# Performance work log

Hardware: AMD Instinct MI355X
Metric: run time of the kernel (lower is better)

The kernel has to match this reference:

```python
import jax, jax.numpy as jnp
import numpy as np

NS = 4  # ns_mesh hard-coded to [4,4,4] in the original forward


def _interp_weights(positions, cell):
    """Order-3 (M3) B-spline interpolation weights and periodic mesh indices.

    Returns w27 (N,27) combined weights and lin (N,27) flat mesh indices.
    """
    frac = positions @ jnp.linalg.inv(cell)          # fractional coords (N,3)
    u = frac * NS
    nearest = jnp.floor(u + 0.5)
    x = u - nearest                                   # in [-0.5, 0.5]
    # order-3 assignment weights at offsets -1, 0, +1
    w = jnp.stack([0.5 * (0.5 - x) ** 2,
                   0.75 - x ** 2,
                   0.5 * (0.5 + x) ** 2], axis=-1)    # (N,3dims,3offs)
    offs = jnp.array([-1, 0, 1], dtype=jnp.int32)
    idx = (nearest[..., None].astype(jnp.int32) + offs) % NS  # (N,3,3)
    w27 = (w[:, 0, :, None, None] * w[:, 1, None, :, None] * w[:, 2, None, None, :]
           ).reshape(-1, 27)
    lin = (idx[:, 0, :, None, None] * NS * NS
           + idx[:, 1, None, :, None] * NS
           + idx[:, 2, None, None, :]).reshape(-1, 27)
    return w27, lin


def _kspace_filter(cell, sigma2):
    """Smeared-Coulomb kernel exp(-k^2 sigma2/2)/k^2 on the rfft half-grid."""
    G = 2.0 * jnp.pi * jnp.linalg.inv(cell).T         # reciprocal lattice rows
    fx = jnp.fft.fftfreq(NS) * NS                     # integer frequencies
    fz = jnp.fft.rfftfreq(NS) * NS
    kvec = (fx[:, None, None, None] * G[0]
            + fx[None, :, None, None] * G[1]
            + fz[None, None, :, None] * G[2])         # (NS,NS,NS//2+1,3)
    k2 = jnp.sum(kvec ** 2, axis=-1)
    k2_safe = jnp.where(k2 > 0, k2, 1.0)
    return jnp.where(k2 > 0, jnp.exp(-k2 * sigma2 * 0.5) / k2_safe, 0.0)


def reference(positions, cell, charges, sigma2, W1, b1, W2, b2, W3, b3):
    w27, lin = _interp_weights(positions, cell)       # (N,27) each
    C = charges.shape[1]
    # points_to_mesh: scatter-add charges with stencil weights
    contrib = (w27[:, :, None] * charges[:, None, :]).reshape(-1, C)
    mesh_flat = jnp.zeros((NS ** 3, C), charges.dtype).at[lin.reshape(-1)].add(contrib)
    mesh = mesh_flat.T.reshape(C, NS, NS, NS)
    # k-space filter: rfft (backward norm) -> multiply -> irfft (forward norm)
    kernel = _kspace_filter(cell, sigma2)
    mesh_hat = jnp.fft.rfftn(mesh, axes=(1, 2, 3))
    mesh = jnp.fft.irfftn(mesh_hat * kernel, s=(NS, NS, NS), axes=(1, 2, 3),
                          norm="forward")
    # mesh_to_points: gather with the same stencil weights
    mesh_flat = mesh.reshape(C, -1).T                 # (NS^3, C)
    pot = jnp.sum(mesh_flat[lin] * w27[:, :, None], axis=1)  # (N,C)
    # tiny MLP on [charge, potential]
    x = jnp.concatenate([charges, pot], axis=1)       # (N,2)
    x = jnp.tanh(x @ W1 + b1)
    x = jnp.tanh(x @ W2 + b2)
    return jnp.sum(x @ W3 + b3)


def setup_inputs() -> dict:
    key = jax.random.key(0)
    ks = jax.random.split(key, 8)
    N = 2_000_000
    L = 6.0
    positions = jax.random.uniform(ks[0], (N, 3), dtype=jnp.float32) * L
    cell = jnp.eye(3, dtype=jnp.float32) * L
    charges = jax.random.normal(ks[1], (N, 1), dtype=jnp.float32)
    sigma2 = jnp.asarray(1.0, dtype=jnp.float32)
    s1, s2, s3 = (1.0 / np.sqrt(2), 1.0 / np.sqrt(10), 1.0 / np.sqrt(10))
    W1 = jax.random.normal(ks[2], (2, 10), jnp.float32) * s1
    b1 = jnp.zeros((10,), jnp.float32)
    W2 = jax.random.normal(ks[3], (10, 10), jnp.float32) * s2
    b2 = jnp.zeros((10,), jnp.float32)
    W3 = jax.random.normal(ks[4], (10, 1), jnp.float32) * s3
    b3 = jnp.zeros((1,), jnp.float32)
    return {"positions": positions, "cell": cell, "charges": charges,
            "sigma2": sigma2, "W1": W1, "b1": b1, "W2": W2, "b2": b2,
            "W3": W3, "b3": b3}
```

## Files before the change

### kernel.cpp

```cpp
#include <hip/hip_runtime.h>
#include <math.h>

#define NSM 4
#define NCELL 64
#define R1_BLOCKS 64

typedef float f32x2 __attribute__((ext_vector_type(2)));

#define TANH_SC 2.8853900817779268f


__device__ __forceinline__ f32x2 splat2(float s) { f32x2 v; v.x = s; v.y = s; return v; }

__device__ __forceinline__ f32x2 pkfma(f32x2 a, f32x2 b, f32x2 c) {
#if __has_builtin(__builtin_elementwise_fma)
    return __builtin_elementwise_fma(a, b, c);
#else
    f32x2 r; r.x = fmaf(a.x, b.x, c.x); r.y = fmaf(a.y, b.y, c.y); return r;
#endif
}

__device__ __forceinline__ float fast_exp2(float x) {
#if __has_builtin(__builtin_amdgcn_exp2f)
    return __builtin_amdgcn_exp2f(x);
#else
    return exp2f(x);
#endif
}

__device__ __forceinline__ void inv3x3(const float* __restrict__ C, float* inv) {
    float a=C[0],b=C[1],c=C[2],d=C[3],e=C[4],f=C[5],g=C[6],h=C[7],i=C[8];
    float A  =  (e*i - f*h);
    float B  = -(d*i - f*g);
    float Cc =  (d*h - e*g);
    float det = a*A + b*B + c*Cc;
    float rd = 1.0f/det;
    inv[0] = A*rd;        inv[1] = (c*h - b*i)*rd; inv[2] = (b*f - c*e)*rd;
    inv[3] = B*rd;        inv[4] = (a*i - c*g)*rd; inv[5] = (c*d - a*f)*rd;
    inv[6] = Cc*rd;       inv[7] = (b*g - a*h)*rd; inv[8] = (a*e - b*d)*rd;
}

struct AxW { float wm, w0, wp; int n; };
__device__ __forceinline__ AxW axw(float u) {
    AxW r;
    float nf = rintf(u);
    float x  = u - nf;
    r.w0 = 0.75f - x*x;
    float tm = 0.5f - x;  r.wm = 0.5f*tm*tm;
    float tp = 0.5f + x;  r.wp = 0.5f*tp*tp;
    r.n = ((int)nf) & 3;
    return r;
}

__device__ __forceinline__ void axis_w4(float u, float* __restrict__ W) {
    AxW a = axw(u);
    #pragma unroll
    for (int j = 0; j < 4; j++) {
        float w = (a.n == j)         ? a.w0 : 0.0f;
        w       = (a.n == ((j+1)&3)) ? a.wm : w;
        w       = (a.n == ((j+3)&3)) ? a.wp : w;
        W[j] = w;
    }
}

__device__ __forceinline__ float tanh1(float x) {
    float e = fast_exp2(x * TANH_SC);
    return fmaf(-2.0f, __builtin_amdgcn_rcpf(e + 1.0f), 1.0f);
}
__device__ __forceinline__ f32x2 tanh2v(f32x2 v) {
    float e0 = fast_exp2(v.x * TANH_SC);
    float e1 = fast_exp2(v.y * TANH_SC);
    f32x2 r;
    r.x = fmaf(-2.0f, __builtin_amdgcn_rcpf(e0 + 1.0f), 1.0f);
    r.y = fmaf(-2.0f, __builtin_amdgcn_rcpf(e1 + 1.0f), 1.0f);
    return r;
}


__device__ __forceinline__ void scatter_one(float px, float py, float pz, float q,
                                            const float* __restrict__ ci,
                                            f32x2* __restrict__ macc) {
    float fx = px*ci[0] + py*ci[3] + pz*ci[6];
    float fy = px*ci[1] + py*ci[4] + pz*ci[7];
    float fz = px*ci[2] + py*ci[5] + pz*ci[8];
    float X[4], Y[4], Z[4];
    axis_w4(fx*(float)NSM, X);
    axis_w4(fy*(float)NSM, Y);
    axis_w4(fz*(float)NSM, Z);
    f32x2 z01; z01.x = Z[0]; z01.y = Z[1];
    f32x2 z23; z23.x = Z[2]; z23.y = Z[3];
    float qX[4];
    #pragma unroll
    for (int x = 0; x < 4; x++) qX[x] = q * X[x];
    #pragma unroll
    for (int x = 0; x < 4; x++) {
        #pragma unroll
        for (int y = 0; y < 4; y++) {
            f32x2 w2 = splat2(qX[x] * Y[y]);
            macc[x*8 + y*2    ] = pkfma(w2, z01, macc[x*8 + y*2    ]);
            macc[x*8 + y*2 + 1] = pkfma(w2, z23, macc[x*8 + y*2 + 1]);
        }
    }
}

__global__ __launch_bounds__(256) void scatter_kernel(
        const float* __restrict__ pos, const float* __restrict__ cell,
        const float* __restrict__ charges, float* __restrict__ partial, int N) {
    __shared__ f32x2 red[128][32];
    __shared__ f32x2 red2[8][32];
    float ci[9]; inv3x3(cell, ci);

    f32x2 macc[32];
    #pragma unroll
    for (int c = 0; c < 32; c++) macc[c] = splat2(0.0f);

    const float4* posv = (const float4*)pos;
    const float4* qv   = (const float4*)charges;
    long b = (long)blockIdx.x * blockDim.x + threadIdx.x;
    long i = b * 4;
    if (i + 3 < N) {
        float4 p0 = posv[3*b], p1 = posv[3*b+1], p2 = posv[3*b+2];
        float4 q4 = qv[b];
        scatter_one(p0.x, p0.y, p0.z, q4.x, ci, macc);
        scatter_one(p0.w, p1.x, p1.y, q4.y, ci, macc);
        scatter_one(p1.z, p1.w, p2.x, q4.z, ci, macc);
        scatter_one(p2.y, p2.z, p2.w, q4.w, ci, macc);
    } else if (i < N) {
        for (long k = i; k < N; k++)
            scatter_one(pos[3*k], pos[3*k+1], pos[3*k+2], charges[k], ci, macc);
    }

    #pragma unroll
    for (int c = 0; c < 32; c++) {
        macc[c].x += __shfl_xor(macc[c].x, 32);
        macc[c].y += __shfl_xor(macc[c].y, 32);
    }
    int t = threadIdx.x;
    int row = (t >> 6) * 32 + (t & 31);
    if ((t & 32) == 0) {
        int sw = t & 31;
        #pragma unroll
        for (int c = 0; c < 32; c++) red[row][c ^ sw] = macc[c];
    }
    __syncthreads();
    {
        int p = t & 31, g = t >> 5;
        f32x2 sum = splat2(0.0f);
        #pragma unroll
        for (int i2 = 0; i2 < 16; i2++) {
            int r = g*16 + i2;
            sum += red[r][p ^ (r & 31)];
        }
        red2[g][p] = sum;
    }
    __syncthreads();
    if (t < NCELL) {
        const float* r2 = (const float*)&red2[0][0];
        int pair = t >> 1, comp = t & 1;
        float s = 0.0f;
        #pragma unroll
        for (int gg = 0; gg < 8; gg++) s += r2[(gg*32 + pair)*2 + comp];
        partial[(long)blockIdx.x * NCELL + t] = s;
    }
}


__global__ __launch_bounds__(256) void reduce_stage1_kernel(
        const float* __restrict__ partial, int nb, float* __restrict__ partial2) {
    __shared__ float acc[4][64];
    int t = threadIdx.x;
    int c = t & 63, g = t >> 6;
    float s = 0.0f;
    for (int r = blockIdx.x + 64*g; r < nb; r += 256)
        s += partial[(long)r * NCELL + c];
    acc[g][c] = s;
    __syncthreads();
    if (t < 64) {
        float v = ((acc[0][t] + acc[1][t]) + acc[2][t]) + acc[3][t];
        partial2[(long)blockIdx.x * NCELL + t] = v;
    }
}


__global__ __launch_bounds__(256) void reduce_filter_kernel(
        const float* __restrict__ partial2,
        const float* __restrict__ cell, const float* __restrict__ sigma2p,
        float* __restrict__ mesh_out) {
    __shared__ float4 redA[16][16];
    __shared__ float mm[64];
    __shared__ float gr[64];
    int t = threadIdx.x;

    int c4 = t & 15, g = t >> 4;
    float4 v = make_float4(0.f, 0.f, 0.f, 0.f);
    const float4* p4 = (const float4*)partial2;
    for (int b = g; b < R1_BLOCKS; b += 16) {
        float4 x = p4[b*16 + c4];
        v.x += x.x; v.y += x.y; v.z += x.z; v.w += x.w;
    }
    redA[g][c4] = v;
    __syncthreads();
    if (t < 16) {
        float4 tot = make_float4(0.f, 0.f, 0.f, 0.f);
        #pragma unroll
        for (int gg = 0; gg < 16; gg++) {
            float4 x = redA[gg][t];
            tot.x += x.x; tot.y += x.y; tot.z += x.z; tot.w += x.w;
        }
        ((float4*)mm)[t] = tot;
    }
    __syncthreads();

    if (t < 64) {
        float ci[9]; inv3x3(cell, ci);
        float s2 = sigma2p[0];
        const float twopi = 6.2831853071795864769f;
        float G0x = twopi*ci[0], G0y = twopi*ci[3], G0z = twopi*ci[6];
        float G1x = twopi*ci[1], G1y = twopi*ci[4], G1z = twopi*ci[7];
        float G2x = twopi*ci[2], G2y = twopi*ci[5], G2z = twopi*ci[8];
        int dx = t >> 4, dy = (t >> 2) & 3, dz = t & 3;
        float acc = 0.0f;
        for (int a = 0; a < 4; a++) {
            float fa = (a < 2) ? (float)a : (float)(a - 4);
            for (int b = 0; b < 4; b++) {
                float fb = (b < 2) ? (float)b : (float)(b - 4);
                for (int c = 0; c < 4; c++) {
                    if ((a | b | c) == 0) continue;
                    float fc = (c < 2) ? (float)c : (float)(c - 4);
                    float kx = fa*G0x + fb*G1x + fc*G2x;
                    float ky = fa*G0y + fb*G1y + fc*G2y;
                    float kz = fa*G0z + fb*G1z + fc*G2z;
                    float k2 = kx*kx + ky*ky + kz*kz;
                    float K  = expf(-k2 * s2 * 0.5f) / k2;
                    int ph = (a*dx + b*dy + c*dz) & 3;
                    float cs = (ph == 0) ? 1.0f : ((ph == 2) ? -1.0f : 0.0f);
                    acc += K * cs;
                }
            }
        }
        gr[t] = acc;
    }
    __syncthreads();
    if (t < 64) {
        int dx = t >> 4, dy = (t >> 2) & 3, dz = t & 3;
        float o = 0.0f;
        for (int s = 0; s < 64; s++) {
            int sx = s >> 4, sy = (s >> 2) & 3, sz = s & 3;
            int d = ((dx - sx) & 3)*16 + ((dy - sy) & 3)*4 + ((dz - sz) & 3);
            o += gr[d] * mm[s];
        }
        mesh_out[t] = o;
    }
}


__device__ __forceinline__ float pot_one(float px, float py, float pz,
                                         const float* __restrict__ ci,
                                         const float* __restrict__ mf) {
    float fx = px*ci[0] + py*ci[3] + pz*ci[6];
    float fy = px*ci[1] + py*ci[4] + pz*ci[7];
    float fz = px*ci[2] + py*ci[5] + pz*ci[8];
    float X[4], Y[4], Z[4];
    axis_w4(fx*(float)NSM, X);
    axis_w4(fy*(float)NSM, Y);
    axis_w4(fz*(float)NSM, Z);
    f32x2 a01 = splat2(0.0f), a23 = splat2(0.0f);
    #pragma unroll
    for (int x = 0; x < 4; x++) {
        #pragma unroll
        for (int y = 0; y < 4; y++) {
            f32x2 w2 = splat2(X[x] * Y[y]);
            f32x2 m01, m23;
            m01.x = mf[x*16 + y*4 + 0]; m01.y = mf[x*16 + y*4 + 1];
            m23.x = mf[x*16 + y*4 + 2]; m23.y = mf[x*16 + y*4 + 3];
            a01 = pkfma(w2, m01, a01);
            a23 = pkfma(w2, m23, a23);
        }
    }
    return a01.x*Z[0] + a01.y*Z[1] + a23.x*Z[2] + a23.y*Z[3];
}

__global__ __launch_bounds__(256, 4) void gather_mlp_kernel(
        const float* __restrict__ pos, const float* __restrict__ cell,
        const float* __restrict__ charges,
        const float* __restrict__ W1, const float* __restrict__ b1,
        const float* __restrict__ W2, const float* __restrict__ b2,
        const float* __restrict__ W3, const float* __restrict__ b3,
        const float* __restrict__ meshf, float* __restrict__ bsum, int N) {
    __shared__ float wavesum[4];
    int t = threadIdx.x;
    float ci[9]; inv3x3(cell, ci);

    long t4 = (long)blockIdx.x * blockDim.x + threadIdx.x;
    long i0 = t4 * 4;
    float ysum = 0.0f;

    if (i0 + 3 < N) {
        const float4* posv = (const float4*)pos;
        float4 p0 = posv[3*t4], p1 = posv[3*t4+1], p2 = posv[3*t4+2];
        float4 q4 = ((const float4*)charges)[t4];

        float pt0 = pot_one(p0.x, p0.y, p0.z, ci, meshf);
        float pt1 = pot_one(p0.w, p1.x, p1.y, ci, meshf);
        float pt2 = pot_one(p1.z, p1.w, p2.x, ci, meshf);
        float pt3 = pot_one(p2.y, p2.z, p2.w, ci, meshf);

        f32x2 q01; q01.x = q4.x; q01.y = q4.y;
        f32x2 q23; q23.x = q4.z; q23.y = q4.w;
        f32x2 pA;  pA.x = pt0;  pA.y = pt1;
        f32x2 pB;  pB.x = pt2;  pB.y = pt3;

        f32x2 h1a[10], h1b[10];
        #pragma unroll
        for (int j = 0; j < 10; j++) {
            f32x2 ta = pkfma(pA, splat2(W1[10 + j]), splat2(b1[j]));
            ta = pkfma(q01, splat2(W1[j]), ta);
            h1a[j] = tanh2v(ta);
            f32x2 tb = pkfma(pB, splat2(W1[10 + j]), splat2(b1[j]));
            tb = pkfma(q23, splat2(W1[j]), tb);
            h1b[j] = tanh2v(tb);
        }
        f32x2 h2a[10], h2b[10];
        #pragma unroll
        for (int j = 0; j < 10; j++) {
            f32x2 aa = splat2(b2[j]), ab = splat2(b2[j]);
            #pragma unroll
            for (int i = 0; i < 10; i++) {
                f32x2 w = splat2(W2[10*i + j]);
                aa = pkfma(h1a[i], w, aa);
                ab = pkfma(h1b[i], w, ab);
            }
            h2a[j] = tanh2v(aa);
            h2b[j] = tanh2v(ab);
        }
        f32x2 ya = splat2(b3[0]), yb = splat2(b3[0]);
        #pragma unroll
        for (int j = 0; j < 10; j++) {
            f32x2 w = splat2(W3[j]);
            ya = pkfma(h2a[j], w, ya);
            yb = pkfma(h2b[j], w, yb);
        }
        ysum = ya.x + ya.y + yb.x + yb.y;
    } else if (i0 < N) {
        for (long k = i0; k < N; k++) {
            float pt = pot_one(pos[3*k], pos[3*k+1], pos[3*k+2], ci, meshf);
            float q  = charges[k];
            float h1[10], h2[10];
            #pragma unroll
            for (int j = 0; j < 10; j++)
                h1[j] = tanh1(fmaf(q, W1[j], fmaf(pt, W1[10 + j], b1[j])));
            #pragma unroll
            for (int j = 0; j < 10; j++) {
                float a2 = b2[j];
                #pragma unroll
                for (int i = 0; i < 10; i++) a2 = fmaf(h1[i], W2[10*i + j], a2);
                h2[j] = tanh1(a2);
            }
            float y = b3[0];
            #pragma unroll
            for (int j = 0; j < 10; j++) y = fmaf(h2[j], W3[j], y);
            ysum += y;
        }
    }

    ysum += __shfl_down(ysum, 32);
    ysum += __shfl_down(ysum, 16);
    ysum += __shfl_down(ysum, 8);
    ysum += __shfl_down(ysum, 4);
    ysum += __shfl_down(ysum, 2);
    ysum += __shfl_down(ysum, 1);
    int wid  = t >> 6;
    int lane = t & 63;
    if (lane == 0) wavesum[wid] = ysum;
    __syncthreads();
    if (t == 0)
        bsum[blockIdx.x] = wavesum[0] + wavesum[1] + wavesum[2] + wavesum[3];
}


__global__ __launch_bounds__(256) void final_sum_kernel(
        const float* __restrict__ bsum, int nb, float* __restrict__ out) {
    __shared__ float wavesum[4];
    float s = 0.0f;
    for (int i = threadIdx.x; i < nb; i += 256) s += bsum[i];
    s += __shfl_down(s, 32);
    s += __shfl_down(s, 16);
    s += __shfl_down(s, 8);
    s += __shfl_down(s, 4);
    s += __shfl_down(s, 2);
    s += __shfl_down(s, 1);
    int wid  = threadIdx.x >> 6;
    int lane = threadIdx.x & 63;
    if (lane == 0) wavesum[wid] = s;
    __syncthreads();
    if (threadIdx.x == 0)
        out[0] = wavesum[0] + wavesum[1] + wavesum[2] + wavesum[3];
}


extern "C" void kernel_launch(void* const* d_in, const int* in_sizes, int n_in,
                              void* d_out, int out_size, void* d_ws, size_t ws_size,
                              hipStream_t stream) {
    const float* pos     = (const float*)d_in[0];
    const float* cell    = (const float*)d_in[1];
    const float* charges = (const float*)d_in[2];
    const float* sigma2  = (const float*)d_in[3];
    const float* W1 = (const float*)d_in[4];
    const float* b1 = (const float*)d_in[5];
    const float* W2 = (const float*)d_in[6];
    const float* b2 = (const float*)d_in[7];
    const float* W3 = (const float*)d_in[8];
    const float* b3 = (const float*)d_in[9];
    int N = in_sizes[2];

    int nblocks = (int)(((long)N + 1023) / 1024);

    float* partial  = (float*)d_ws;
    float* partial2 = partial + (long)nblocks * NCELL;
    float* meshf    = partial2 + (long)R1_BLOCKS * NCELL;
    float* bsum     = meshf + NCELL;

    scatter_kernel<<<nblocks, 256, 0, stream>>>(pos, cell, charges, partial, N);
    reduce_stage1_kernel<<<R1_BLOCKS, 256, 0, stream>>>(partial, nblocks, partial2);
    reduce_filter_kernel<<<1, 256, 0, stream>>>(partial2, cell, sigma2, meshf);
    gather_mlp_kernel<<<nblocks, 256, 0, stream>>>(pos, cell, charges,
                                                   W1, b1, W2, b2, W3, b3,
                                                   meshf, bsum, N);
    final_sum_kernel<<<1, 256, 0, stream>>>(bsum, nblocks, (float*)d_out);
}
```

Before: 54.83 us.

## Halve scatter blocks and fuse two-stage partial reduction into filter kernel

The scatter kernel now processes two groups of four points per thread through a grid-stride loop. This halves the number of per-block partial meshes. The separate reduce_stage1 kernel is removed, and a single 1024-thread block sums the partials directly, computing the k-space Green's function in parallel on another wavefront. This removes one kernel launch and an intermediate buffer round trip. The cost is that one block serially reduces about a thousand partial rows, and each scatter thread runs longer.

```diff
diff --git a/kernel.cpp b/kernel.cpp
--- a/kernel.cpp
+++ b/kernel.cpp
@@ -3,7 +3,6 @@
 
 #define NSM 4
 #define NCELL 64
-#define R1_BLOCKS 64
 
 typedef float f32x2 __attribute__((ext_vector_type(2)));
 
@@ -116,18 +115,25 @@
 
     const float4* posv = (const float4*)pos;
     const float4* qv   = (const float4*)charges;
-    long b = (long)blockIdx.x * blockDim.x + threadIdx.x;
-    long i = b * 4;
-    if (i + 3 < N) {
-        float4 p0 = posv[3*b], p1 = posv[3*b+1], p2 = posv[3*b+2];
-        float4 q4 = qv[b];
-        scatter_one(p0.x, p0.y, p0.z, q4.x, ci, macc);
-        scatter_one(p0.w, p1.x, p1.y, q4.y, ci, macc);
-        scatter_one(p1.z, p1.w, p2.x, q4.z, ci, macc);
-        scatter_one(p2.y, p2.z, p2.w, q4.w, ci, macc);
-    } else if (i < N) {
-        for (long k = i; k < N; k++)
-            scatter_one(pos[3*k], pos[3*k+1], pos[3*k+2], charges[k], ci, macc);
+    long NB4    = ((long)N + 3) / 4;
+    long stride = (long)gridDim.x * blockDim.x;
+
+    #pragma unroll
+    for (int pass = 0; pass < 2; pass++) {
+        long b = (long)blockIdx.x * blockDim.x + threadIdx.x + pass * stride;
+        if (b >= NB4) break;
+        long i = b * 4;
+        if (i + 3 < N) {
+            float4 p0 = posv[3*b], p1 = posv[3*b+1], p2 = posv[3*b+2];
+            float4 q4 = qv[b];
+            scatter_one(p0.x, p0.y, p0.z, q4.x, ci, macc);
+            scatter_one(p0.w, p1.x, p1.y, q4.y, ci, macc);
+            scatter_one(p1.z, p1.w, p2.x, q4.z, ci, macc);
+            scatter_one(p2.y, p2.z, p2.w, q4.w, ci, macc);
+        } else {
+            for (long k = i; k < N; k++)
+                scatter_one(pos[3*k], pos[3*k+1], pos[3*k+2], charges[k], ci, macc);
+        }
     }
 
     #pragma unroll
@@ -165,89 +171,66 @@
 }
 
 
-__global__ __launch_bounds__(256) void reduce_stage1_kernel(
-        const float* __restrict__ partial, int nb, float* __restrict__ partial2) {
-    __shared__ float acc[4][64];
-    int t = threadIdx.x;
-    int c = t & 63, g = t >> 6;
-    float s = 0.0f;
-    for (int r = blockIdx.x + 64*g; r < nb; r += 256)
-        s += partial[(long)r * NCELL + c];
-    acc[g][c] = s;
-    __syncthreads();
-    if (t < 64) {
-        float v = ((acc[0][t] + acc[1][t]) + acc[2][t]) + acc[3][t];
-        partial2[(long)blockIdx.x * NCELL + t] = v;
-    }
-}
-
-
-__global__ __launch_bounds__(256) void reduce_filter_kernel(
-        const float* __restrict__ partial2,
+__global__ __launch_bounds__(1024) void reduce_filter_kernel(
+        const float* __restrict__ partial, int nb,
         const float* __restrict__ cell, const float* __restrict__ sigma2p,
         float* __restrict__ mesh_out) {
-    __shared__ float4 redA[16][16];
+    __shared__ float acc[16][64];
     __shared__ float mm[64];
     __shared__ float gr[64];
     int t = threadIdx.x;
-
-    int c4 = t & 15, g = t >> 4;
-    float4 v = make_float4(0.f, 0.f, 0.f, 0.f);
-    const float4* p4 = (const float4*)partial2;
-    for (int b = g; b < R1_BLOCKS; b += 16) {
-        float4 x = p4[b*16 + c4];
-        v.x += x.x; v.y += x.y; v.z += x.z; v.w += x.w;
-    }
-    redA[g][c4] = v;
-    __syncthreads();
-    if (t < 16) {
-        float4 tot = make_float4(0.f, 0.f, 0.f, 0.f);
-        #pragma unroll
-        for (int gg = 0; gg < 16; gg++) {
-            float4 x = redA[gg][t];
-            tot.x += x.x; tot.y += x.y; tot.z += x.z; tot.w += x.w;
-        }
-        ((float4*)mm)[t] = tot;
-    }
-    __syncthreads();
-
-    if (t < 64) {
+    int c = t & 63, g = t >> 6;
+
+    float s = 0.0f;
+    for (int r = g; r < nb; r += 16)
+        s += partial[(long)r * NCELL + c];
+    acc[g][c] = s;
+
+    if (t >= 64 && t < 128) {
+        int tt = t - 64;
         float ci[9]; inv3x3(cell, ci);
         float s2 = sigma2p[0];
         const float twopi = 6.2831853071795864769f;
         float G0x = twopi*ci[0], G0y = twopi*ci[3], G0z = twopi*ci[6];
         float G1x = twopi*ci[1], G1y = twopi*ci[4], G1z = twopi*ci[7];
         float G2x = twopi*ci[2], G2y = twopi*ci[5], G2z = twopi*ci[8];
-        int dx = t >> 4, dy = (t >> 2) & 3, dz = t & 3;
-        float acc = 0.0f;
+        int dx = tt >> 4, dy = (tt >> 2) & 3, dz = tt & 3;
+        float accg = 0.0f;
         for (int a = 0; a < 4; a++) {
             float fa = (a < 2) ? (float)a : (float)(a - 4);
             for (int b = 0; b < 4; b++) {
                 float fb = (b < 2) ? (float)b : (float)(b - 4);
-                for (int c = 0; c < 4; c++) {
-                    if ((a | b | c) == 0) continue;
-                    float fc = (c < 2) ? (float)c : (float)(c - 4);
+                for (int cc = 0; cc < 4; cc++) {
+                    if ((a | b | cc) == 0) continue;
+                    float fc = (cc < 2) ? (float)cc : (float)(cc - 4);
                     float kx = fa*G0x + fb*G1x + fc*G2x;
                     float ky = fa*G0y + fb*G1y + fc*G2y;
                     float kz = fa*G0z + fb*G1z + fc*G2z;
                     float k2 = kx*kx + ky*ky + kz*kz;
                     float K  = expf(-k2 * s2 * 0.5f) / k2;
-                    int ph = (a*dx + b*dy + c*dz) & 3;
+                    int ph = (a*dx + b*dy + cc*dz) & 3;
                     float cs = (ph == 0) ? 1.0f : ((ph == 2) ? -1.0f : 0.0f);
-                    acc += K * cs;
+                    accg += K * cs;
                 }
             }
         }
-        gr[t] = acc;
+        gr[tt] = accg;
+    }
+    __syncthreads();
+    if (t < 64) {
+        float v = 0.0f;
+        #pragma unroll
+        for (int gg = 0; gg < 16; gg++) v += acc[gg][t];
+        mm[t] = v;
     }
     __syncthreads();
     if (t < 64) {
         int dx = t >> 4, dy = (t >> 2) & 3, dz = t & 3;
         float o = 0.0f;
-        for (int s = 0; s < 64; s++) {
-            int sx = s >> 4, sy = (s >> 2) & 3, sz = s & 3;
+        for (int s2i = 0; s2i < 64; s2i++) {
+            int sx = s2i >> 4, sy = (s2i >> 2) & 3, sz = s2i & 3;
             int d = ((dx - sx) & 3)*16 + ((dy - sy) & 3)*4 + ((dz - sz) & 3);
-            o += gr[d] * mm[s];
+            o += gr[d] * mm[s2i];
         }
         mesh_out[t] = o;
     }
@@ -413,18 +396,18 @@
     const float* b3 = (const float*)d_in[9];
     int N = in_sizes[2];
 
-    int nblocks = (int)(((long)N + 1023) / 1024);
-
-    float* partial  = (float*)d_ws;
-    float* partial2 = partial + (long)nblocks * NCELL;
-    float* meshf    = partial2 + (long)R1_BLOCKS * NCELL;
-    float* bsum     = meshf + NCELL;
-
-    scatter_kernel<<<nblocks, 256, 0, stream>>>(pos, cell, charges, partial, N);
-    reduce_stage1_kernel<<<R1_BLOCKS, 256, 0, stream>>>(partial, nblocks, partial2);
-    reduce_filter_kernel<<<1, 256, 0, stream>>>(partial2, cell, sigma2, meshf);
-    gather_mlp_kernel<<<nblocks, 256, 0, stream>>>(pos, cell, charges,
-                                                   W1, b1, W2, b2, W3, b3,
-                                                   meshf, bsum, N);
-    final_sum_kernel<<<1, 256, 0, stream>>>(bsum, nblocks, (float*)d_out);
-}
+    int sc_blocks = (int)(((long)N + 2047) / 2048);
+    int ga_blocks = (int)(((long)N + 1023) / 1024);
+
+    float* partial = (float*)d_ws;
+    float* meshf   = partial + (long)sc_blocks * NCELL;
+    float* bsum    = meshf + NCELL;
+
+    scatter_kernel<<<sc_blocks, 256, 0, stream>>>(pos, cell, charges, partial, N);
+    reduce_filter_kernel<<<1, 1024, 0, stream>>>(partial, sc_blocks,
+                                                 cell, sigma2, meshf);
+    gather_mlp_kernel<<<ga_blocks, 256, 0, stream>>>(pos, cell, charges,
+                                                     W1, b1, W2, b2, W3, b3,
+                                                     meshf, bsum, N);
+    final_sum_kernel<<<1, 256, 0, stream>>>(bsum, ga_blocks, (float*)d_out);
+}
```

New measurement: 64.40 us. +17.5%, slower.
